# Kernel optimization log

Hardware: AMD Instinct MI355X
Metric: run time of the kernel (lower is better)

The kernel has to match this reference:

```python
import jax, jax.numpy as jnp
import numpy as np

B = 4
NV = 6890           # SMPL vertex count
NF0 = 13776         # SMPL face count (before fill_back)
T = 3               # tex_size
IMG = 128           # render image size
UVH = UVW = 256     # uv image resolution
FLENGTH = 500.0
NEAR, FAR = 0.1, 25.0
CHUNK = 128         # faces per z-buffer scan step
BIG = jnp.float32(1e10)


def setup_inputs():
    key = jax.random.key(0)
    ks = jax.random.split(key, 5)
    faces0 = jax.random.randint(ks[0], (NF0, 3), 0, NV, dtype=jnp.int32)
    faces = jnp.concatenate([faces0, faces0[:, ::-1]], axis=0)  # fill_back
    cam = jnp.concatenate([0.8 + 0.2 * jax.random.uniform(ks[1], (B, 1)),
                           0.05 * jax.random.normal(ks[2], (B, 2))], axis=1)
    vertices = 0.3 * jax.random.normal(ks[3], (B, NV, 3))
    uv_imgs = jax.random.uniform(ks[4], (B, 3, UVH, UVW))
    img2uv_sampler = jax.random.uniform(jax.random.fold_in(key, 7),
                                        (faces.shape[0], T * T, 2)) * 2.0 - 1.0
    return {"cam": cam, "vertices": vertices, "uv_imgs": uv_imgs,
            "img2uv_sampler": img2uv_sampler, "faces": faces}


def _grid_sample(img, grid):
    # img (B,C,H,W), grid (B,N,2) xy in [-1,1]; bilinear, align_corners=False, zeros padding
    Bc, C, H, W = img.shape
    x = (grid[..., 0] + 1.0) * (W * 0.5) - 0.5
    y = (grid[..., 1] + 1.0) * (H * 0.5) - 0.5
    x0f = jnp.floor(x); y0f = jnp.floor(y)
    wx = x - x0f; wy = y - y0f
    x0 = x0f.astype(jnp.int32); y0 = y0f.astype(jnp.int32)
    imgf = img.reshape(Bc, C, H * W)
    def gat(yi, xi, w):
        valid = (xi >= 0) & (xi < W) & (yi >= 0) & (yi < H)
        idx = jnp.clip(yi, 0, H - 1) * W + jnp.clip(xi, 0, W - 1)
        v = jax.vmap(lambda im, i: im[:, i])(imgf, idx)  # (B,C,N)
        return v * (w * valid)[:, None, :]
    return (gat(y0, x0, (1 - wx) * (1 - wy)) + gat(y0, x0 + 1, wx * (1 - wy)) +
            gat(y0 + 1, x0, (1 - wx) * wy) + gat(y0 + 1, x0 + 1, wx * wy))


def _extract_tex(uv_imgs, sampler, nf):
    # sampler (B,nf,T*T,2) -> textures (B,nf,T,T,T,3)
    tex = _grid_sample(uv_imgs, sampler.reshape(uv_imgs.shape[0], -1, 2))
    tex = tex.reshape(-1, 3, nf, T, T).transpose(0, 2, 3, 4, 1)  # (B,nf,T,T,3)
    return jnp.broadcast_to(tex[:, :, :, :, None, :], tex.shape[:4] + (T, 3))


def _lighting(face_verts, textures):
    # module defaults: ambient intensity 1, directional 0, white lights, dir=(0,1,0)
    v0, v1, v2 = face_verts[:, :, 0], face_verts[:, :, 1], face_verts[:, :, 2]
    n = jnp.cross(v1 - v0, v2 - v0)
    n = n / (jnp.linalg.norm(n, axis=-1, keepdims=True) + 1e-10)
    cos = jnp.maximum(n @ jnp.array([0.0, 1.0, 0.0]), 0.0)       # (B,F)
    light = 1.0 * jnp.ones(3) + 0.0 * cos[..., None] * jnp.ones(3)  # (B,F,3)
    return textures * light[:, :, None, None, None, :]


def _weak_projection(cam, vertices):
    p = IMG / 2.0
    tz = FLENGTH / (p * cam[:, 0:1])                              # (B,1)
    v2d = cam[:, None, 0:1] * (vertices[:, :, :2] + cam[:, None, 1:])
    return jnp.concatenate([v2d, vertices[:, :, 2:3] + tz[:, None, :]], axis=-1)


def _bary(fv, px, py):
    # fv: (...,3,3) triangle screen verts; px,py broadcastable pixel coords
    x0 = fv[..., 0, 0]; y0 = fv[..., 0, 1]
    x1 = fv[..., 1, 0]; y1 = fv[..., 1, 1]
    x2 = fv[..., 2, 0]; y2 = fv[..., 2, 1]
    w0 = (x2 - x1) * (py - y1) - (y2 - y1) * (px - x1)
    w1 = (x0 - x2) * (py - y2) - (y0 - y2) * (px - x2)
    w2 = (x1 - x0) * (py - y0) - (y1 - y0) * (px - x0)
    area = w0 + w1 + w2
    s = jnp.where(area == 0, 1.0, area)
    return w0 / s, w1 / s, w2 / s, area


def _pixel_grid():
    xs = (2.0 * jnp.arange(IMG) + 1.0) / IMG - 1.0                # (W,)
    ys = (1.0 - (2.0 * jnp.arange(IMG) + 1.0) / IMG)[:, None]     # (H,1), +y up
    return xs, ys


def _rasterize_fim(face_verts):
    # face_verts (B,F,3,3) in screen coords -> face index map (B,H,W), -1 = bg
    Bc, F = face_verts.shape[:2]
    pad = (-F) % CHUNK
    fv = jnp.pad(face_verts, ((0, 0), (0, pad), (0, 0), (0, 0)))
    S = (F + pad) // CHUNK
    fv = fv.reshape(Bc, S, CHUNK, 3, 3).transpose(1, 0, 2, 3, 4)  # (S,B,C,3,3)
    xs, ys = _pixel_grid()
    def step(carry, inp):
        zbuf, fim = carry
        f, base = inp
        fe = f[:, :, None, None, :, :]                            # (B,C,1,1,3,3)
        b0, b1, b2, area = _bary(fe, xs, ys)                      # (B,C,H,W)
        z0 = f[:, :, 0, 2][..., None, None]
        z1 = f[:, :, 1, 2][..., None, None]
        z2 = f[:, :, 2, 2][..., None, None]
        invz = b0 / z0 + b1 / z1 + b2 / z2                        # perspective-correct
        zp = 1.0 / jnp.where(invz == 0, 1.0, invz)
        inside = (b0 >= 0) & (b1 >= 0) & (b2 >= 0) & (area > 0)   # front-facing only
        valid = inside & (zp > NEAR) & (zp < FAR)
        depth = jnp.where(valid, zp, BIG)
        dmin = jnp.min(depth, axis=1)                             # (B,H,W)
        amin = jnp.argmin(depth, axis=1).astype(jnp.int32) + base
        better = dmin < zbuf
        return (jnp.where(better, dmin, zbuf),
                jnp.where(better, amin, fim)), None
    zbuf0 = jnp.full((Bc, IMG, IMG), BIG)
    fim0 = jnp.full((Bc, IMG, IMG), -1, jnp.int32)
    bases = (jnp.arange(S) * CHUNK).astype(jnp.int32)
    (zbuf, fim), _ = jax.lax.scan(step, (zbuf0, fim0), (fv, bases))
    return fim


def _shade(face_verts, textures, fim):
    # nearest-texel barycentric texture lookup, as in neural_renderer forward
    Bc, F = face_verts.shape[:2]
    fid = jnp.clip(fim, 0, F - 1).reshape(Bc, -1)                 # (B,HW)
    fv = jax.vmap(lambda v, i: v[i])(face_verts, fid)             # (B,HW,3,3)
    fv = fv.reshape(Bc, IMG, IMG, 3, 3)
    xs, ys = _pixel_grid()
    b0, b1, b2, _ = _bary(fv, xs, ys)                             # (B,H,W)
    t0 = jnp.clip(jnp.floor(b0 * T).astype(jnp.int32), 0, T - 1)
    t1 = jnp.clip(jnp.floor(b1 * T).astype(jnp.int32), 0, T - 1)
    t2 = jnp.clip(jnp.floor(b2 * T).astype(jnp.int32), 0, T - 1)
    idx = ((jnp.clip(fim, 0, F - 1) * T + t0) * T + t1) * T + t2  # (B,H,W)
    texf = textures.reshape(Bc, F * T * T * T, 3)
    col = jax.vmap(lambda t, i: t[i])(texf, idx.reshape(Bc, -1))  # (B,HW,3)
    col = col.reshape(Bc, IMG, IMG, 3)
    col = jnp.where((fim >= 0)[..., None], col, 0.0)              # bg color (0,0,0)
    return col.transpose(0, 3, 1, 2)                              # (B,3,H,W)


def reference(cam, vertices, uv_imgs, img2uv_sampler, faces):
    Bc = cam.shape[0]
    nf = faces.shape[0]
    sampler = jnp.broadcast_to(img2uv_sampler[None], (Bc,) + img2uv_sampler.shape)
    textures = _extract_tex(uv_imgs, sampler, nf)                 # (B,nf,T,T,T,3)
    textures = _lighting(vertices[:, faces], textures)
    verts_p = _weak_projection(cam, vertices)
    fv = verts_p[:, faces]                                        # (B,nf,3,3)
    fv_sg = jax.lax.stop_gradient(fv)  # hard rasterization is non-differentiable
    fim = _rasterize_fim(fv_sg)
    images = _shade(fv_sg, textures, fim)
    return images


if __name__ == "__main__":
    out = reference(**setup_inputs())
    print(out.shape, out.dtype)
```

## Files before the change

kernel.cpp:

```cpp
#include <hip/hip_runtime.h>
#include <stdint.h>

#pragma clang fp contract(off)

#define B_    4
#define NV_   6890
#define NF_   27552
#define IMG_  128
#define UV_   256
#define NPIX  (IMG_*IMG_)

#define TS_     8
#define TPB_    (IMG_/TS_)
#define NTILE_  (TPB_*TPB_)
#define NBIN_   (B_*NTILE_)
#define LIST_CAP (2*1024*1024)
#define MAXC_   (LIST_CAP/256 + NBIN_)

__global__ void __launch_bounds__(256) project_k(
    const float* __restrict__ cam, const float* __restrict__ verts,
    float* __restrict__ vp) {
  int idx = blockIdx.x * 256 + threadIdx.x;
  if (idx >= B_ * NV_) return;
  int b = idx / NV_;
  float c0 = cam[b * 3 + 0], c1 = cam[b * 3 + 1], c2 = cam[b * 3 + 2];
  float tz = 500.0f / (64.0f * c0);
  const float* src = verts + (size_t)idx * 3;
  float* dst = vp + (size_t)idx * 3;
  dst[0] = c0 * (src[0] + c1);
  dst[1] = c0 * (src[1] + c2);
  dst[2] = src[2] + tz;
}

__device__ __forceinline__ int face_tiles(
    const float* __restrict__ vp, const int* __restrict__ faces, int b, int f,
    int& tx0, int& tx1, int& ty0, int& ty1) {
  int ia = faces[f * 3 + 0], ib = faces[f * 3 + 1], ic = faces[f * 3 + 2];
  const float* vb = vp + (size_t)b * NV_ * 3;
  float x0 = vb[ia * 3 + 0], y0 = vb[ia * 3 + 1];
  float x1 = vb[ib * 3 + 0], y1 = vb[ib * 3 + 1];
  float x2 = vb[ic * 3 + 0], y2 = vb[ic * 3 + 1];
  float area_c = (x1 - x0) * (y2 - y0) - (y1 - y0) * (x2 - x0);
  if (area_c < -1e-3f) return 0;
  float xmn = fminf(x0, fminf(x1, x2)), xmx = fmaxf(x0, fmaxf(x1, x2));
  float ymn = fminf(y0, fminf(y1, y2)), ymx = fmaxf(y0, fmaxf(y1, y2));
  int jlo = (int)floorf((xmn + 1.0f) * 64.0f - 0.5f) - 1;
  int jhi = (int)ceilf ((xmx + 1.0f) * 64.0f - 0.5f) + 1;
  int ilo = (int)floorf((1.0f - ymx) * 64.0f - 0.5f) - 1;
  int ihi = (int)ceilf ((1.0f - ymn) * 64.0f - 0.5f) + 1;
  if (jhi < 0 || ihi < 0 || jlo > IMG_ - 1 || ilo > IMG_ - 1) return 0;
  jlo = max(jlo, 0); ilo = max(ilo, 0);
  jhi = min(jhi, IMG_ - 1); ihi = min(ihi, IMG_ - 1);
  tx0 = jlo >> 3; tx1 = jhi >> 3; ty0 = ilo >> 3; ty1 = ihi >> 3;
  return 1;
}

__global__ void __launch_bounds__(256) bin_count_k(
    const float* __restrict__ vp, const int* __restrict__ faces,
    int* __restrict__ cnt, int* __restrict__ rects) {
  __shared__ int scnt[NTILE_];
  int f = blockIdx.x * 256 + threadIdx.x;
  int b = blockIdx.y;
  scnt[threadIdx.x] = 0;
  __syncthreads();
  int tx0, tx1, ty0, ty1;
  int valid = (f < NF_) ? face_tiles(vp, faces, b, f, tx0, tx1, ty0, ty1) : 0;
  if (f < NF_)
    rects[(size_t)b * NF_ + f] =
        valid ? (tx0 | (tx1 << 4) | (ty0 << 8) | (ty1 << 12) | (1 << 16)) : 0;
  if (valid)
    for (int ty = ty0; ty <= ty1; ++ty)
      for (int tx = tx0; tx <= tx1; ++tx)
        atomicAdd(&scnt[ty * TPB_ + tx], 1);
  __syncthreads();
  int t = threadIdx.x;
  int v = scnt[t];
  if (v > 0) atomicAdd(&cnt[b * NTILE_ + t], v);
}

__global__ void __launch_bounds__(1024) scan_k(
    const int* __restrict__ cnt, int* __restrict__ off, int* __restrict__ cur,
    int* __restrict__ work, int* __restrict__ nC) {
  __shared__ int sm[NBIN_];
  int t = threadIdx.x;
  int v = cnt[t];
  sm[t] = v;
  __syncthreads();
  for (int d = 1; d < NBIN_; d <<= 1) {
    int u = (t >= d) ? sm[t - d] : 0;
    __syncthreads();
    sm[t] += u;
    __syncthreads();
  }
  int o = sm[t] - v;
  off[t] = o;
  cur[t] = o;
  int nch = (v + 255) >> 8;
  __syncthreads();
  sm[t] = nch;
  __syncthreads();
  for (int d = 1; d < NBIN_; d <<= 1) {
    int u = (t >= d) ? sm[t - d] : 0;
    __syncthreads();
    sm[t] += u;
    __syncthreads();
  }
  int cb = sm[t] - nch;
  if (t == NBIN_ - 1) nC[0] = sm[t];
  for (int c = 0; c < nch; ++c) work[cb + c] = t | (c << 10);
}

__global__ void __launch_bounds__(256) bin_fill_k(
    const int* __restrict__ rects, int* __restrict__ cur,
    int* __restrict__ list) {
  __shared__ int scnt[NTILE_];
  __shared__ int sbase[NTILE_];
  int f = blockIdx.x * 256 + threadIdx.x;
  int b = blockIdx.y;
  scnt[threadIdx.x] = 0;
  __syncthreads();
  int rv = (f < NF_) ? rects[(size_t)b * NF_ + f] : 0;
  int valid = rv >> 16;
  int tx0 = rv & 15, tx1 = (rv >> 4) & 15;
  int ty0 = (rv >> 8) & 15, ty1 = (rv >> 12) & 15;
  if (valid)
    for (int ty = ty0; ty <= ty1; ++ty)
      for (int tx = tx0; tx <= tx1; ++tx)
        atomicAdd(&scnt[ty * TPB_ + tx], 1);
  __syncthreads();
  int t = threadIdx.x;
  int v = scnt[t];
  if (v > 0) sbase[t] = atomicAdd(&cur[b * NTILE_ + t], v);
  __syncthreads();
  scnt[t] = 0;
  __syncthreads();
  if (valid)
    for (int ty = ty0; ty <= ty1; ++ty)
      for (int tx = tx0; tx <= tx1; ++tx) {
        int bin = ty * TPB_ + tx;
        int r = atomicAdd(&scnt[bin], 1);
        int slot = sbase[bin] + r;
        if (slot < LIST_CAP) list[slot] = f;
      }
}

__global__ void __launch_bounds__(256) raster_k(
    const float* __restrict__ vp, const int* __restrict__ faces,
    const int* __restrict__ list, const int* __restrict__ cnt,
    const int* __restrict__ off, const int* __restrict__ work,
    const int* __restrict__ nC, unsigned long long* __restrict__ zkey) {
  __shared__ float4 fd[4][5][64];
  __shared__ unsigned long long mg[4][64];
  int bid = blockIdx.x;
  if (bid >= nC[0]) return;
  int wkv = work[bid];
  int bin = wkv & (NBIN_ - 1);
  int chunk = wkv >> 10;
  int b = bin >> 8;
  int t = bin & 255;
  int tyT = t >> 4, txT = t & 15;
  int ws = threadIdx.x >> 6, lane = threadIdx.x & 63;
  int pi = tyT * TS_ + (lane >> 3);
  int pj = txT * TS_ + (lane & 7);
  float px = fmaf((float)pj, 0.015625f, -0.9921875f);
  float py = fmaf((float)pi, -0.015625f, 0.9921875f);

  int n = cnt[bin];
  int seg = (chunk << 8) + (ws << 6);
  int base0 = off[bin] + seg;
  int mw = min(n - seg, 64);
  mw = max(mw, 0);

  if (lane < mw) {
    int fid = list[base0 + lane];
    int ia = faces[fid * 3 + 0], ib = faces[fid * 3 + 1],
        ic = faces[fid * 3 + 2];
    const float* vb = vp + (size_t)b * NV_ * 3;
    float X0 = vb[ia * 3 + 0], Y0 = vb[ia * 3 + 1], Z0 = vb[ia * 3 + 2];
    float X1 = vb[ib * 3 + 0], Y1 = vb[ib * 3 + 1], Z1 = vb[ib * 3 + 2];
    float X2 = vb[ic * 3 + 0], Y2 = vb[ic * 3 + 1], Z2 = vb[ic * 3 + 2];
    fd[ws][0][lane] = make_float4(X2 - X1, Y2 - Y1, X1, Y1);
    fd[ws][1][lane] = make_float4(X0 - X2, Y0 - Y2, X2, Y2);
    fd[ws][2][lane] = make_float4(X1 - X0, Y1 - Y0, X0, Y0);
    fd[ws][3][lane] = make_float4(Z0, Z1, Z2, __int_as_float(fid));
    fd[ws][4][lane] =
        make_float4(Z1 * Z2, Z0 * Z2, Z0 * Z1, Z0 * Z1 * Z2);
  }
  __syncthreads();

  unsigned long long kb = ~0ull;
  float gate = __uint_as_float(0xFFFFFFFFu);
  for (int q = 0; q < mw; ++q) {
    float4 A = fd[ws][0][q];
    float4 Bv = fd[ws][1][q];
    float4 Cv = fd[ws][2][q];
    float w0 = A.x * (py - A.w) - A.y * (px - A.z);
    float w1 = Bv.x * (py - Bv.w) - Bv.y * (px - Bv.z);
    float w2 = Cv.x * (py - Cv.w) - Cv.y * (px - Cv.z);
    float area = (w0 + w1) + w2;
    float mn = fminf(w0, fminf(w1, w2));
    if (area > 0.0f && !(mn < 0.0f)) {
      float4 P = fd[ws][4][q];
      float num = (w0 * P.x + w1 * P.y) + w2 * P.z;
      float zpa = (area * P.w) * __builtin_amdgcn_rcpf(num);
      if (!(zpa > gate)) {
        float4 Z = fd[ws][3][q];
        float b0 = w0 / area, b1 = w1 / area, b2 = w2 / area;
        float invz = (b0 / Z.x + b1 / Z.y) + b2 / Z.z;
        float zp = 1.0f / (invz == 0.0f ? 1.0f : invz);
        if (zp > 0.1f && zp < 25.0f) {
          unsigned long long key =
              ((unsigned long long)__float_as_uint(zp) << 32) |
              (unsigned int)__float_as_int(Z.w);
          if (key < kb) {
            kb = key;
            gate = __uint_as_float((unsigned int)(kb >> 32)) * 1.001f;
          }
        }
      }
    }
  }

  mg[ws][lane] = kb;
  __syncthreads();
  if (ws == 0) {
    unsigned long long k0 = mg[0][lane];
    unsigned long long k1 = mg[1][lane];
    unsigned long long k2 = mg[2][lane];
    unsigned long long k3 = mg[3][lane];
    k0 = k1 < k0 ? k1 : k0;
    k2 = k3 < k2 ? k3 : k2;
    k0 = k2 < k0 ? k2 : k0;
    if (k0 != ~0ull)
      atomicMin(zkey + (size_t)b * NPIX + pi * IMG_ + pj, k0);
  }
}

#define TAP(ty, tx, wexpr)                                                   \
  {                                                                          \
    int ty_ = (ty), tx_ = (tx);                                              \
    float w_ = (wexpr);                                                      \
    float valid_ =                                                           \
        (tx_ >= 0 && tx_ < UV_ && ty_ >= 0 && ty_ < UV_) ? 1.0f : 0.0f;      \
    float wv_ = w_ * valid_;                                                 \
    int cy_ = min(max(ty_, 0), UV_ - 1), cx_ = min(max(tx_, 0), UV_ - 1);    \
    int o_ = cy_ * UV_ + cx_;                                                \
    cr = cr + img[o_] * wv_;                                                 \
    cg = cg + img[UV_ * UV_ + o_] * wv_;                                     \
    cb = cb + img[2 * UV_ * UV_ + o_] * wv_;                                 \
  }

__global__ void __launch_bounds__(256) shade_k(
    const float* __restrict__ vp, const int* __restrict__ faces,
    const float* __restrict__ uv, const float* __restrict__ samp,
    const unsigned long long* __restrict__ zkey, float* __restrict__ out) {
  int idx = blockIdx.x * 256 + threadIdx.x;
  if (idx >= B_ * NPIX) return;
  int b = idx / NPIX;
  int p = idx - b * NPIX;
  int ii = p / IMG_;
  int jj = p - ii * IMG_;

  unsigned long long key = zkey[idx];
  float cr = 0.0f, cg = 0.0f, cb = 0.0f;
  if (key != 0xFFFFFFFFFFFFFFFFull) {
    int f = (int)(key & 0xFFFFFFFFull);
    int ia = faces[f * 3 + 0], ib = faces[f * 3 + 1], ic = faces[f * 3 + 2];
    const float* vb = vp + (size_t)b * NV_ * 3;
    float x0 = vb[ia * 3 + 0], y0 = vb[ia * 3 + 1];
    float x1 = vb[ib * 3 + 0], y1 = vb[ib * 3 + 1];
    float x2 = vb[ic * 3 + 0], y2 = vb[ic * 3 + 1];
    float px = (float)(2 * jj + 1) / 128.0f - 1.0f;
    float py = 1.0f - (float)(2 * ii + 1) / 128.0f;
    float w0 = (x2 - x1) * (py - y1) - (y2 - y1) * (px - x1);
    float w1 = (x0 - x2) * (py - y2) - (y0 - y2) * (px - x2);
    float w2 = (x1 - x0) * (py - y0) - (y1 - y0) * (px - x0);
    float area = (w0 + w1) + w2;
    float s = (area == 0.0f) ? 1.0f : area;
    float b0 = w0 / s, b1 = w1 / s;
    int t0 = min(max((int)floorf(b0 * 3.0f), 0), 2);
    int t1 = min(max((int)floorf(b1 * 3.0f), 0), 2);

    const float* g = samp + ((size_t)f * 9 + (size_t)(t0 * 3 + t1)) * 2;
    float gx = g[0], gy = g[1];
    float x = (gx + 1.0f) * 128.0f - 0.5f;
    float y = (gy + 1.0f) * 128.0f - 0.5f;
    float x0f = floorf(x), y0f = floorf(y);
    float wx = x - x0f, wy = y - y0f;
    int xi = (int)x0f, yi = (int)y0f;
    float omwx = 1.0f - wx, omwy = 1.0f - wy;
    const float* img = uv + (size_t)b * 3 * UV_ * UV_;
    TAP(yi,     xi,     omwx * omwy)
    TAP(yi,     xi + 1, wx * omwy)
    TAP(yi + 1, xi,     omwx * wy)
    TAP(yi + 1, xi + 1, wx * wy)
  }
  out[((size_t)b * 3 + 0) * NPIX + p] = cr;
  out[((size_t)b * 3 + 1) * NPIX + p] = cg;
  out[((size_t)b * 3 + 2) * NPIX + p] = cb;
}

extern "C" void kernel_launch(void* const* d_in, const int* in_sizes, int n_in,
                              void* d_out, int out_size, void* d_ws,
                              size_t ws_size, hipStream_t stream) {
  const float* cam   = (const float*)d_in[0];
  const float* verts = (const float*)d_in[1];
  const float* uv    = (const float*)d_in[2];
  const float* samp  = (const float*)d_in[3];
  const int*   faces = (const int*)d_in[4];

  char* ws = (char*)d_ws;
  size_t o = 0;
  unsigned long long* zkey = (unsigned long long*)(ws + o);
  o += (size_t)B_ * NPIX * 8;
  float* vp = (float*)(ws + o);
  o += ((size_t)B_ * NV_ * 3 * 4 + 1023) & ~1023ull;
  int* cnt   = (int*)(ws + o); o += NBIN_ * 4;
  int* offs  = (int*)(ws + o); o += NBIN_ * 4;
  int* cur   = (int*)(ws + o); o += NBIN_ * 4;
  int* nC    = (int*)(ws + o); o += 1024;
  int* work  = (int*)(ws + o); o += (size_t)MAXC_ * 4;
  int* rects = (int*)(ws + o); o += (size_t)B_ * NF_ * 4;
  int* list  = (int*)(ws + o);

  hipMemsetAsync(zkey, 0xFF, (size_t)B_ * NPIX * 8, stream);
  hipMemsetAsync(cnt, 0, NBIN_ * 4, stream);
  project_k<<<(B_ * NV_ + 255) / 256, 256, 0, stream>>>(cam, verts, vp);
  dim3 bgrid((NF_ + 255) / 256, B_);
  bin_count_k<<<bgrid, 256, 0, stream>>>(vp, faces, cnt, rects);
  scan_k<<<1, NBIN_, 0, stream>>>(cnt, offs, cur, work, nC);
  bin_fill_k<<<bgrid, 256, 0, stream>>>(rects, cur, list);
  raster_k<<<MAXC_, 256, 0, stream>>>(vp, faces, list, cnt, offs, work, nC,
                                      zkey);
  shade_k<<<(B_ * NPIX + 255) / 256, 256, 0, stream>>>(vp, faces, uv, samp,
                                                       zkey, (float*)d_out);
}
```

Baseline: 213.4 us.

## Bucket binned faces by depth and stop rasterizing tiles once depth is resolved

Faces are binned per tile into 16 depth buckets, using the per-batch z range computed during projection. Each raster block then owns a whole tile and walks the buckets from near to far. It stops as soon as every pixel's current nearest depth is in front of the next bucket's lower edge. The chunked work list, the zkey memset and the global atomicMin on zkey are replaced by a direct store. In exchange, each tile is processed serially by one block, which reduces parallelism, and binning now uses global atomics per cell.

```diff
diff --git a/kernel.cpp b/kernel.cpp
--- a/kernel.cpp
+++ b/kernel.cpp
@@ -14,27 +14,41 @@
 #define TPB_    (IMG_/TS_)
 #define NTILE_  (TPB_*TPB_)
 #define NBIN_   (B_*NTILE_)
-#define LIST_CAP (2*1024*1024)
-#define MAXC_   (LIST_CAP/256 + NBIN_)
+#define NBKT_   16
+#define NCELL_  (NBIN_*NBKT_)
+#define LIST_CAP 1835008
 
 __global__ void __launch_bounds__(256) project_k(
     const float* __restrict__ cam, const float* __restrict__ verts,
-    float* __restrict__ vp) {
+    float* __restrict__ vp, unsigned* __restrict__ zmn,
+    unsigned* __restrict__ zmx) {
+  __shared__ unsigned smn[B_], smx[B_];
   int idx = blockIdx.x * 256 + threadIdx.x;
-  if (idx >= B_ * NV_) return;
-  int b = idx / NV_;
-  float c0 = cam[b * 3 + 0], c1 = cam[b * 3 + 1], c2 = cam[b * 3 + 2];
-  float tz = 500.0f / (64.0f * c0);
-  const float* src = verts + (size_t)idx * 3;
-  float* dst = vp + (size_t)idx * 3;
-  dst[0] = c0 * (src[0] + c1);
-  dst[1] = c0 * (src[1] + c2);
-  dst[2] = src[2] + tz;
+  if (threadIdx.x < B_) { smn[threadIdx.x] = 0xFFFFFFFFu; smx[threadIdx.x] = 0u; }
+  __syncthreads();
+  if (idx < B_ * NV_) {
+    int b = idx / NV_;
+    float c0 = cam[b * 3 + 0], c1 = cam[b * 3 + 1], c2 = cam[b * 3 + 2];
+    float tz = 500.0f / (64.0f * c0);
+    const float* src = verts + (size_t)idx * 3;
+    float* dst = vp + (size_t)idx * 3;
+    dst[0] = c0 * (src[0] + c1);
+    dst[1] = c0 * (src[1] + c2);
+    float z = src[2] + tz;
+    dst[2] = z;
+    atomicMin(&smn[b], __float_as_uint(z));
+    atomicMax(&smx[b], __float_as_uint(z));
+  }
+  __syncthreads();
+  if (threadIdx.x < B_) {
+    atomicMin(&zmn[threadIdx.x], smn[threadIdx.x]);
+    atomicMax(&zmx[threadIdx.x], smx[threadIdx.x]);
+  }
 }
 
 __device__ __forceinline__ int face_tiles(
     const float* __restrict__ vp, const int* __restrict__ faces, int b, int f,
-    int& tx0, int& tx1, int& ty0, int& ty1) {
+    int& tx0, int& tx1, int& ty0, int& ty1, float& zminF) {
   int ia = faces[f * 3 + 0], ib = faces[f * 3 + 1], ic = faces[f * 3 + 2];
   const float* vb = vp + (size_t)b * NV_ * 3;
   float x0 = vb[ia * 3 + 0], y0 = vb[ia * 3 + 1];
@@ -52,39 +66,48 @@
   jlo = max(jlo, 0); ilo = max(ilo, 0);
   jhi = min(jhi, IMG_ - 1); ihi = min(ihi, IMG_ - 1);
   tx0 = jlo >> 3; tx1 = jhi >> 3; ty0 = ilo >> 3; ty1 = ihi >> 3;
+  float z0 = vb[ia * 3 + 2], z1 = vb[ib * 3 + 2], z2 = vb[ic * 3 + 2];
+  zminF = fminf(z0, fminf(z1, z2));
   return 1;
 }
 
 __global__ void __launch_bounds__(256) bin_count_k(
     const float* __restrict__ vp, const int* __restrict__ faces,
-    int* __restrict__ cnt, int* __restrict__ rects) {
-  __shared__ int scnt[NTILE_];
+    const unsigned* __restrict__ zmn, const unsigned* __restrict__ zmx,
+    int* __restrict__ cntq, int* __restrict__ rects) {
   int f = blockIdx.x * 256 + threadIdx.x;
   int b = blockIdx.y;
-  scnt[threadIdx.x] = 0;
-  __syncthreads();
-  int tx0, tx1, ty0, ty1;
-  int valid = (f < NF_) ? face_tiles(vp, faces, b, f, tx0, tx1, ty0, ty1) : 0;
-  if (f < NF_)
-    rects[(size_t)b * NF_ + f] =
-        valid ? (tx0 | (tx1 << 4) | (ty0 << 8) | (ty1 << 12) | (1 << 16)) : 0;
+  if (f >= NF_) return;
+  int tx0, tx1, ty0, ty1; float zf;
+  int valid = face_tiles(vp, faces, b, f, tx0, tx1, ty0, ty1, zf);
+  int q = 0;
+  if (valid) {
+    float zlo = __uint_as_float(zmn[b]);
+    float zhi = __uint_as_float(zmx[b]);
+    float sc = 16.0f / (zhi - zlo);
+    q = (int)((zf - zlo) * sc);
+    q = min(NBKT_ - 1, max(0, q));
+  }
+  rects[(size_t)b * NF_ + f] =
+      valid ? (tx0 | (tx1 << 4) | (ty0 << 8) | (ty1 << 12) | (1 << 16) |
+               (q << 17))
+            : 0;
   if (valid)
     for (int ty = ty0; ty <= ty1; ++ty)
       for (int tx = tx0; tx <= tx1; ++tx)
-        atomicAdd(&scnt[ty * TPB_ + tx], 1);
-  __syncthreads();
-  int t = threadIdx.x;
-  int v = scnt[t];
-  if (v > 0) atomicAdd(&cnt[b * NTILE_ + t], v);
+        atomicAdd(&cntq[(((b * NTILE_) + ty * TPB_ + tx) << 4) + q], 1);
 }
 
 __global__ void __launch_bounds__(1024) scan_k(
-    const int* __restrict__ cnt, int* __restrict__ off, int* __restrict__ cur,
-    int* __restrict__ work, int* __restrict__ nC) {
+    const int* __restrict__ cntq, int* __restrict__ offq,
+    int* __restrict__ cur) {
   __shared__ int sm[NBIN_];
   int t = threadIdx.x;
-  int v = cnt[t];
-  sm[t] = v;
+  int base = t * NBKT_;
+  int loc[NBKT_];
+  int tot = 0;
+  for (int i = 0; i < NBKT_; ++i) { loc[i] = tot; tot += cntq[base + i]; }
+  sm[t] = tot;
   __syncthreads();
   for (int d = 1; d < NBIN_; d <<= 1) {
     int u = (t >= d) ? sm[t - d] : 0;
@@ -92,70 +115,42 @@
     sm[t] += u;
     __syncthreads();
   }
-  int o = sm[t] - v;
-  off[t] = o;
-  cur[t] = o;
-  int nch = (v + 255) >> 8;
-  __syncthreads();
-  sm[t] = nch;
-  __syncthreads();
-  for (int d = 1; d < NBIN_; d <<= 1) {
-    int u = (t >= d) ? sm[t - d] : 0;
-    __syncthreads();
-    sm[t] += u;
-    __syncthreads();
-  }
-  int cb = sm[t] - nch;
-  if (t == NBIN_ - 1) nC[0] = sm[t];
-  for (int c = 0; c < nch; ++c) work[cb + c] = t | (c << 10);
+  int pre = sm[t] - tot;
+  for (int i = 0; i < NBKT_; ++i) {
+    int o = pre + loc[i];
+    offq[base + i] = o;
+    cur[base + i] = o;
+  }
 }
 
 __global__ void __launch_bounds__(256) bin_fill_k(
     const int* __restrict__ rects, int* __restrict__ cur,
     int* __restrict__ list) {
-  __shared__ int scnt[NTILE_];
-  __shared__ int sbase[NTILE_];
   int f = blockIdx.x * 256 + threadIdx.x;
   int b = blockIdx.y;
-  scnt[threadIdx.x] = 0;
-  __syncthreads();
-  int rv = (f < NF_) ? rects[(size_t)b * NF_ + f] : 0;
-  int valid = rv >> 16;
+  if (f >= NF_) return;
+  int rv = rects[(size_t)b * NF_ + f];
+  if (!(rv & (1 << 16))) return;
   int tx0 = rv & 15, tx1 = (rv >> 4) & 15;
   int ty0 = (rv >> 8) & 15, ty1 = (rv >> 12) & 15;
-  if (valid)
-    for (int ty = ty0; ty <= ty1; ++ty)
-      for (int tx = tx0; tx <= tx1; ++tx)
-        atomicAdd(&scnt[ty * TPB_ + tx], 1);
-  __syncthreads();
-  int t = threadIdx.x;
-  int v = scnt[t];
-  if (v > 0) sbase[t] = atomicAdd(&cur[b * NTILE_ + t], v);
-  __syncthreads();
-  scnt[t] = 0;
-  __syncthreads();
-  if (valid)
-    for (int ty = ty0; ty <= ty1; ++ty)
-      for (int tx = tx0; tx <= tx1; ++tx) {
-        int bin = ty * TPB_ + tx;
-        int r = atomicAdd(&scnt[bin], 1);
-        int slot = sbase[bin] + r;
-        if (slot < LIST_CAP) list[slot] = f;
-      }
+  int q = (rv >> 17) & 15;
+  for (int ty = ty0; ty <= ty1; ++ty)
+    for (int tx = tx0; tx <= tx1; ++tx) {
+      int cell = (((b * NTILE_) + ty * TPB_ + tx) << 4) + q;
+      int slot = atomicAdd(&cur[cell], 1);
+      if (slot < LIST_CAP) list[slot] = f;
+    }
 }
 
 __global__ void __launch_bounds__(256) raster_k(
     const float* __restrict__ vp, const int* __restrict__ faces,
-    const int* __restrict__ list, const int* __restrict__ cnt,
-    const int* __restrict__ off, const int* __restrict__ work,
-    const int* __restrict__ nC, unsigned long long* __restrict__ zkey) {
+    const int* __restrict__ list, const int* __restrict__ cntq,
+    const int* __restrict__ offq, const unsigned* __restrict__ zmn,
+    const unsigned* __restrict__ zmx, unsigned long long* __restrict__ zkey) {
   __shared__ float4 fd[4][5][64];
+  __shared__ unsigned long long pmin[64];
   __shared__ unsigned long long mg[4][64];
-  int bid = blockIdx.x;
-  if (bid >= nC[0]) return;
-  int wkv = work[bid];
-  int bin = wkv & (NBIN_ - 1);
-  int chunk = wkv >> 10;
+  int bin = blockIdx.x;
   int b = bin >> 8;
   int t = bin & 255;
   int tyT = t >> 4, txT = t & 15;
@@ -164,76 +159,99 @@
   int pj = txT * TS_ + (lane & 7);
   float px = fmaf((float)pj, 0.015625f, -0.9921875f);
   float py = fmaf((float)pi, -0.015625f, 0.9921875f);
-
-  int n = cnt[bin];
-  int seg = (chunk << 8) + (ws << 6);
-  int base0 = off[bin] + seg;
-  int mw = min(n - seg, 64);
-  mw = max(mw, 0);
-
-  if (lane < mw) {
-    int fid = list[base0 + lane];
-    int ia = faces[fid * 3 + 0], ib = faces[fid * 3 + 1],
-        ic = faces[fid * 3 + 2];
-    const float* vb = vp + (size_t)b * NV_ * 3;
-    float X0 = vb[ia * 3 + 0], Y0 = vb[ia * 3 + 1], Z0 = vb[ia * 3 + 2];
-    float X1 = vb[ib * 3 + 0], Y1 = vb[ib * 3 + 1], Z1 = vb[ib * 3 + 2];
-    float X2 = vb[ic * 3 + 0], Y2 = vb[ic * 3 + 1], Z2 = vb[ic * 3 + 2];
-    fd[ws][0][lane] = make_float4(X2 - X1, Y2 - Y1, X1, Y1);
-    fd[ws][1][lane] = make_float4(X0 - X2, Y0 - Y2, X2, Y2);
-    fd[ws][2][lane] = make_float4(X1 - X0, Y1 - Y0, X0, Y0);
-    fd[ws][3][lane] = make_float4(Z0, Z1, Z2, __int_as_float(fid));
-    fd[ws][4][lane] =
-        make_float4(Z1 * Z2, Z0 * Z2, Z0 * Z1, Z0 * Z1 * Z2);
-  }
+  float zlo = __uint_as_float(zmn[b]);
+  float bw16 = (__uint_as_float(zmx[b]) - zlo) * 0.0625f;
+  if (threadIdx.x < 64) pmin[threadIdx.x] = ~0ull;
   __syncthreads();
 
-  unsigned long long kb = ~0ull;
-  float gate = __uint_as_float(0xFFFFFFFFu);
-  for (int q = 0; q < mw; ++q) {
-    float4 A = fd[ws][0][q];
-    float4 Bv = fd[ws][1][q];
-    float4 Cv = fd[ws][2][q];
-    float w0 = A.x * (py - A.w) - A.y * (px - A.z);
-    float w1 = Bv.x * (py - Bv.w) - Bv.y * (px - Bv.z);
-    float w2 = Cv.x * (py - Cv.w) - Cv.y * (px - Cv.z);
-    float area = (w0 + w1) + w2;
-    float mn = fminf(w0, fminf(w1, w2));
-    if (area > 0.0f && !(mn < 0.0f)) {
-      float4 P = fd[ws][4][q];
-      float num = (w0 * P.x + w1 * P.y) + w2 * P.z;
-      float zpa = (area * P.w) * __builtin_amdgcn_rcpf(num);
-      if (!(zpa > gate)) {
-        float4 Z = fd[ws][3][q];
-        float b0 = w0 / area, b1 = w1 / area, b2 = w2 / area;
-        float invz = (b0 / Z.x + b1 / Z.y) + b2 / Z.z;
-        float zp = 1.0f / (invz == 0.0f ? 1.0f : invz);
-        if (zp > 0.1f && zp < 25.0f) {
-          unsigned long long key =
-              ((unsigned long long)__float_as_uint(zp) << 32) |
-              (unsigned int)__float_as_int(Z.w);
-          if (key < kb) {
-            kb = key;
-            gate = __uint_as_float((unsigned int)(kb >> 32)) * 1.001f;
+  for (int q = 0; q < NBKT_; ++q) {
+    unsigned long long kb = pmin[lane];
+    if (q > 0) {
+      unsigned kz = (unsigned)(kb >> 32);
+      for (int d = 1; d < 64; d <<= 1) {
+        unsigned o = (unsigned)__shfl_xor((int)kz, d, 64);
+        kz = kz > o ? kz : o;
+      }
+      if (kz != 0xFFFFFFFFu) {
+        float edge = fmaf((float)q, bw16, zlo);
+        if (__uint_as_float(kz) < edge - 1e-3f) break;
+      }
+    }
+    int cell = (bin << 4) + q;
+    int nq = cntq[cell];
+    if (nq == 0) continue;
+    int base = offq[cell];
+    float gate = __uint_as_float((unsigned)(kb >> 32)) * 1.001f;
+
+    int nbat = (nq + 255) >> 8;
+    for (int s = 0; s < nbat; ++s) {
+      int seg = (s << 8) + (ws << 6);
+      int mw = min(nq - seg, 64);
+      if (mw > 0) {
+        if (lane < mw) {
+          int fid = list[base + seg + lane];
+          int ia = faces[fid * 3 + 0], ib = faces[fid * 3 + 1],
+              ic = faces[fid * 3 + 2];
+          const float* vb = vp + (size_t)b * NV_ * 3;
+          float X0 = vb[ia * 3 + 0], Y0 = vb[ia * 3 + 1], Z0 = vb[ia * 3 + 2];
+          float X1 = vb[ib * 3 + 0], Y1 = vb[ib * 3 + 1], Z1 = vb[ib * 3 + 2];
+          float X2 = vb[ic * 3 + 0], Y2 = vb[ic * 3 + 1], Z2 = vb[ic * 3 + 2];
+          fd[ws][0][lane] = make_float4(X2 - X1, Y2 - Y1, X1, Y1);
+          fd[ws][1][lane] = make_float4(X0 - X2, Y0 - Y2, X2, Y2);
+          fd[ws][2][lane] = make_float4(X1 - X0, Y1 - Y0, X0, Y0);
+          fd[ws][3][lane] = make_float4(Z0, Z1, Z2, __int_as_float(fid));
+          fd[ws][4][lane] =
+              make_float4(Z1 * Z2, Z0 * Z2, Z0 * Z1, Z0 * Z1 * Z2);
+        }
+        for (int k = 0; k < mw; ++k) {
+          float4 A = fd[ws][0][k];
+          float4 Bv = fd[ws][1][k];
+          float4 Cv = fd[ws][2][k];
+          float w0 = A.x * (py - A.w) - A.y * (px - A.z);
+          float w1 = Bv.x * (py - Bv.w) - Bv.y * (px - Bv.z);
+          float w2 = Cv.x * (py - Cv.w) - Cv.y * (px - Cv.z);
+          float area = (w0 + w1) + w2;
+          float mn = fminf(w0, fminf(w1, w2));
+          if (area > 0.0f && !(mn < 0.0f)) {
+            float4 P = fd[ws][4][k];
+            float num = (w0 * P.x + w1 * P.y) + w2 * P.z;
+            float zpa = (area * P.w) * __builtin_amdgcn_rcpf(num);
+            if (!(zpa > gate)) {
+              float4 Z = fd[ws][3][k];
+              float b0 = w0 / area, b1 = w1 / area, b2 = w2 / area;
+              float invz = (b0 / Z.x + b1 / Z.y) + b2 / Z.z;
+              float zp = 1.0f / (invz == 0.0f ? 1.0f : invz);
+              if (zp > 0.1f && zp < 25.0f) {
+                unsigned long long key =
+                    ((unsigned long long)__float_as_uint(zp) << 32) |
+                    (unsigned int)__float_as_int(Z.w);
+                if (key < kb) {
+                  kb = key;
+                  gate = __uint_as_float((unsigned)(kb >> 32)) * 1.001f;
+                }
+              }
+            }
           }
         }
       }
     }
-  }
-
-  mg[ws][lane] = kb;
-  __syncthreads();
-  if (ws == 0) {
-    unsigned long long k0 = mg[0][lane];
-    unsigned long long k1 = mg[1][lane];
-    unsigned long long k2 = mg[2][lane];
-    unsigned long long k3 = mg[3][lane];
-    k0 = k1 < k0 ? k1 : k0;
-    k2 = k3 < k2 ? k3 : k2;
-    k0 = k2 < k0 ? k2 : k0;
-    if (k0 != ~0ull)
-      atomicMin(zkey + (size_t)b * NPIX + pi * IMG_ + pj, k0);
-  }
+    mg[ws][lane] = kb;
+    __syncthreads();
+    if (ws == 0) {
+      unsigned long long k0 = mg[0][lane];
+      unsigned long long k1 = mg[1][lane];
+      unsigned long long k2 = mg[2][lane];
+      unsigned long long k3 = mg[3][lane];
+      k0 = k1 < k0 ? k1 : k0;
+      k2 = k3 < k2 ? k3 : k2;
+      k0 = k2 < k0 ? k2 : k0;
+      unsigned long long p = pmin[lane];
+      pmin[lane] = k0 < p ? k0 : p;
+    }
+    __syncthreads();
+  }
+  if (ws == 0)
+    zkey[(size_t)b * NPIX + pi * IMG_ + pj] = pmin[lane];
 }
 
 #define TAP(ty, tx, wexpr)                                                   \
@@ -315,22 +333,24 @@
   o += (size_t)B_ * NPIX * 8;
   float* vp = (float*)(ws + o);
   o += ((size_t)B_ * NV_ * 3 * 4 + 1023) & ~1023ull;
-  int* cnt   = (int*)(ws + o); o += NBIN_ * 4;
-  int* offs  = (int*)(ws + o); o += NBIN_ * 4;
-  int* cur   = (int*)(ws + o); o += NBIN_ * 4;
-  int* nC    = (int*)(ws + o); o += 1024;
-  int* work  = (int*)(ws + o); o += (size_t)MAXC_ * 4;
-  int* rects = (int*)(ws + o); o += (size_t)B_ * NF_ * 4;
+  int* cntq = (int*)(ws + o); o += NCELL_ * 4;
+  int* offq = (int*)(ws + o); o += NCELL_ * 4;
+  int* cur  = (int*)(ws + o); o += NCELL_ * 4;
+  unsigned* zmn = (unsigned*)(ws + o); o += 512;
+  unsigned* zmx = (unsigned*)(ws + o); o += 512;
+  int* rects = (int*)(ws + o); o += ((size_t)B_ * NF_ * 4 + 1023) & ~1023ull;
   int* list  = (int*)(ws + o);
 
-  hipMemsetAsync(zkey, 0xFF, (size_t)B_ * NPIX * 8, stream);
-  hipMemsetAsync(cnt, 0, NBIN_ * 4, stream);
-  project_k<<<(B_ * NV_ + 255) / 256, 256, 0, stream>>>(cam, verts, vp);
+  hipMemsetAsync(cntq, 0, NCELL_ * 4, stream);
+  hipMemsetAsync(zmn, 0xFF, B_ * 4, stream);
+  hipMemsetAsync(zmx, 0x00, B_ * 4, stream);
+  project_k<<<(B_ * NV_ + 255) / 256, 256, 0, stream>>>(cam, verts, vp, zmn,
+                                                        zmx);
   dim3 bgrid((NF_ + 255) / 256, B_);
-  bin_count_k<<<bgrid, 256, 0, stream>>>(vp, faces, cnt, rects);
-  scan_k<<<1, NBIN_, 0, stream>>>(cnt, offs, cur, work, nC);
+  bin_count_k<<<bgrid, 256, 0, stream>>>(vp, faces, zmn, zmx, cntq, rects);
+  scan_k<<<1, NBIN_, 0, stream>>>(cntq, offq, cur);
   bin_fill_k<<<bgrid, 256, 0, stream>>>(rects, cur, list);
-  raster_k<<<MAXC_, 256, 0, stream>>>(vp, faces, list, cnt, offs, work, nC,
+  raster_k<<<NBIN_, 256, 0, stream>>>(vp, faces, list, cntq, offq, zmn, zmx,
                                       zkey);
   shade_k<<<(B_ * NPIX + 255) / 256, 256, 0, stream>>>(vp, faces, uv, samp,
                                                        zkey, (float*)d_out);
```

Result: slower. 573.9 us (+169.0%).
